# Kernel tuning notes

Hardware: AMD Instinct MI355X
Metric: run time of the kernel (lower is better)

Reference implementation:

```python
import jax, jax.numpy as jnp
import numpy as np

N_EXPERTS = 64
TOPK = 4
DIM = 2048
B_T = 8192


def setup_inputs() -> dict:
    key = jax.random.key(0)
    k1, k2 = jax.random.split(key)
    x = jax.random.normal(k1, (B_T, DIM), jnp.float32)
    W = jax.random.normal(k2, (N_EXPERTS, DIM), jnp.float32) * 0.02  # nn.Linear weight (out, in)
    router_bias = jnp.zeros((N_EXPERTS,), jnp.float32)  # registered buffer, init zeros
    return {"x": x, "W": W, "router_bias": router_bias, "token_capacity": 3072}


def _route(x, W, router_bias, token_capacity):
    """Faithful serial greedy capacity-aware routing.

    Replicates the torch nested loop (k-major, token-minor order):
      - per step, pick argmax over the token's (mutated) logits among experts
        with remaining capacity;
      - full experts whose logit exceeds the chosen one get permanently set
        to -inf in that token's logit row (exactly what the inner while-style
        loop does);
      - if no expert has capacity, selected stays -1, weight 0, and the whole
        row becomes -inf (torch sets the top expert to -inf n_experts times).
    """
    logits0 = x @ W.T + router_bias                       # (N, E)
    scores = jax.nn.softmax(logits0, axis=-1)             # (N, E)
    cap = token_capacity // TOPK                          # python int
    remaining0 = jnp.full((N_EXPERTS,), float(cap), jnp.float32)
    N = x.shape[0]
    NEG = jnp.float32(-jnp.inf)

    def step(carry, i):
        logits, remaining = carry
        b = i % N                                         # token index (k-major order)
        row = logits[b]                                   # (E,)
        masked = jnp.where(remaining > 0, row, NEG)
        chosen = jnp.argmax(masked)
        ok = remaining[chosen] > 0                        # False only if all experts full
        sel = jnp.where(ok, chosen, -1).astype(jnp.int32)
        w = jnp.where(ok, scores[b, chosen], jnp.float32(0.0))
        full = remaining <= 0
        cval = row[chosen]
        # full experts 'above' the chosen one were visited and zapped to -inf
        new_row = jnp.where(ok,
                            jnp.where(full & (row > cval), NEG, row),
                            jnp.full_like(row, NEG))
        logits = logits.at[b].set(new_row)
        remaining = remaining.at[chosen].add(jnp.where(ok, jnp.float32(-1.0), jnp.float32(0.0)))
        return (logits, remaining), (sel, w)

    (_, _), (sel_f, w_f) = jax.lax.scan(step, (logits0, remaining0),
                                        jnp.arange(TOPK * N))
    selected = sel_f.reshape(TOPK, N).T                   # (N, TOPK)
    weights = w_f.reshape(TOPK, N).T                      # (N, TOPK)
    weights = weights / (weights.sum(axis=-1, keepdims=True) + 1e-8)
    return selected, weights


def reference(x, W, router_bias, token_capacity):
    return _route(x, W, router_bias, token_capacity)
```

## Files before the change

### kernel.cpp

```cpp
#include <hip/hip_runtime.h>
#include <math.h>

#define N_TOK 8192
#define DIM   2048
#define NE    64
#define TOPK  4
#define THETA 2e-3f
#define TPB2  16
#define NBLK  (N_TOK / TPB2)
#define RSTR  260

typedef short bf16x8 __attribute__((ext_vector_type(8)));
typedef float f32x4  __attribute__((ext_vector_type(4)));

#define OFF_LOGITS 0
#define OFF_MAXV   (OFF_LOGITS + N_TOK * NE)
#define OFF_DENOM  (OFF_MAXV + N_TOK)
#define OFF_W1     (OFF_DENOM + N_TOK)
#define OFF_C1     (OFF_W1 + N_TOK)
#define OFF_NFLAG  (OFF_C1 + N_TOK)
#define OFF_FLAGL  (OFF_NFLAG + 64)
#define OFF_WH     (OFF_FLAGL + N_TOK)
#define OFF_WL     (OFF_WH + NE * DIM / 2)
#define OFF_WT     (OFF_WL + NE * DIM / 2)
#define OFF_WTMP   (OFF_WT + NE * DIM)

__device__ inline void cvt2(float a, float b, unsigned& hi, unsigned& lo) {
    const unsigned ua = __float_as_uint(a), ub = __float_as_uint(b);
    hi = __builtin_amdgcn_perm(ub, ua, 0x07060302u);
    const float ra = a - __uint_as_float(ua & 0xFFFF0000u);
    const float rb = b - __uint_as_float(ub & 0xFFFF0000u);
    lo = __builtin_amdgcn_perm(__float_as_uint(rb), __float_as_uint(ra), 0x07060302u);
}

union FragU { unsigned u[4]; bf16x8 v; uint4 q; };

__device__ inline void make_frags(const float4& p, const float4& q,
                                  bf16x8& hi, bf16x8& lo) {
    FragU H, L;
    cvt2(p.x, p.y, H.u[0], L.u[0]);
    cvt2(p.z, p.w, H.u[1], L.u[1]);
    cvt2(q.x, q.y, H.u[2], L.u[2]);
    cvt2(q.z, q.w, H.u[3], L.u[3]);
    hi = H.v; lo = L.v;
}

__global__ __launch_bounds__(256)
void k_wc(const float* __restrict__ W, unsigned short* __restrict__ wh2,
          unsigned short* __restrict__ wl2, float* __restrict__ wt,
          int* __restrict__ nflag) {
    const int t = blockIdx.x * 256 + threadIdx.x;
    if (t == 0) nflag[0] = 0;
    const int l  = t & 63;
    const int grp = t >> 6;
    const int nt = grp & 3;
    const int kc = grp >> 2;
    const int e  = nt * 16 + (l & 15);
    const int k0 = kc * 32 + (l >> 4) * 8;

    const float4 p = *reinterpret_cast<const float4*>(W + (size_t)e * DIM + k0);
    const float4 q = *reinterpret_cast<const float4*>(W + (size_t)e * DIM + k0 + 4);
    FragU H, L;
    cvt2(p.x, p.y, H.u[0], L.u[0]);
    cvt2(p.z, p.w, H.u[1], L.u[1]);
    cvt2(q.x, q.y, H.u[2], L.u[2]);
    cvt2(q.z, q.w, H.u[3], L.u[3]);
    const size_t off = (size_t)grp * 512 + l * 8;
    *reinterpret_cast<uint4*>(wh2 + off) = H.q;
    *reinterpret_cast<uint4*>(wl2 + off) = L.q;

    wt[(size_t)(k0 + 0) * NE + e] = p.x;
    wt[(size_t)(k0 + 1) * NE + e] = p.y;
    wt[(size_t)(k0 + 2) * NE + e] = p.z;
    wt[(size_t)(k0 + 3) * NE + e] = p.w;
    wt[(size_t)(k0 + 4) * NE + e] = q.x;
    wt[(size_t)(k0 + 5) * NE + e] = q.y;
    wt[(size_t)(k0 + 6) * NE + e] = q.z;
    wt[(size_t)(k0 + 7) * NE + e] = q.w;
}

__global__ __launch_bounds__(512, 4)
void k_main(const float* __restrict__ x, const unsigned short* __restrict__ wh2,
            const unsigned short* __restrict__ wl2, const float* __restrict__ bias,
            float* __restrict__ logits, float* __restrict__ maxv,
            float* __restrict__ denomv, float* __restrict__ w1f,
            int* __restrict__ c1, int* __restrict__ nflag, int* __restrict__ flagl) {
    __shared__ __align__(16) float xs[2][TPB2 * RSTR];
    __shared__ float red[8][TPB2][68];
    __shared__ float lbuf[TPB2][68];

    const int tid = threadIdx.x;
    const int w   = tid >> 6;
    const int l   = tid & 63;
    const int t0  = blockIdx.x * TPB2;
    const int m   = l & 15;
    const int g   = l >> 4;

    const float* xrow0 = x + (size_t)(t0 + 2 * w) * DIM + l * 4;
    const float* xrow1 = x + (size_t)(t0 + 2 * w + 1) * DIM + l * 4;
    float* st0 = &xs[0][(2 * w) * RSTR + l * 4];
    float* st1 = &xs[0][(2 * w + 1) * RSTR + l * 4];
    const int xs1off = TPB2 * RSTR;

    const unsigned short* bh = wh2 + (size_t)w * 2048 + l * 8;
    const unsigned short* bl = wl2 + (size_t)w * 2048 + l * 8;

    f32x4 accA[4], accB[4];
    #pragma unroll
    for (int nt = 0; nt < 4; ++nt)
        #pragma unroll
        for (int r = 0; r < 4; ++r) { accA[nt][r] = 0.0f; accB[nt][r] = 0.0f; }

    {
        const float4 r0 = *reinterpret_cast<const float4*>(xrow0);
        const float4 r1 = *reinterpret_cast<const float4*>(xrow1);
        *reinterpret_cast<float4*>(st0) = r0;
        *reinterpret_cast<float4*>(st1) = r1;
    }
    uint4 BH[2][4], BL[2][4];
    #pragma unroll
    for (int nt = 0; nt < 4; ++nt) {
        BH[0][nt] = *reinterpret_cast<const uint4*>(bh + nt * 512);
        BL[0][nt] = *reinterpret_cast<const uint4*>(bl + nt * 512);
    }
    __syncthreads();

    const int aoff = m * RSTR + w * 32 + g * 8;

    #pragma unroll
    for (int win = 0; win < 8; ++win) {
        const int cur = win & 1, nxt = cur ^ 1;
        float4 nx0, nx1;
        if (win < 7) {
            nx0 = *reinterpret_cast<const float4*>(xrow0 + (win + 1) * 256);
            nx1 = *reinterpret_cast<const float4*>(xrow1 + (win + 1) * 256);
            #pragma unroll
            for (int nt = 0; nt < 4; ++nt) {
                BH[nxt][nt] = *reinterpret_cast<const uint4*>(
                    bh + (size_t)(win + 1) * 16384 + nt * 512);
                BL[nxt][nt] = *reinterpret_cast<const uint4*>(
                    bl + (size_t)(win + 1) * 16384 + nt * 512);
            }
        }

        const float4 p = *reinterpret_cast<const float4*>(&xs[0][cur * xs1off + aoff]);
        const float4 q = *reinterpret_cast<const float4*>(&xs[0][cur * xs1off + aoff + 4]);
        bf16x8 ah, al;
        make_frags(p, q, ah, al);

        #pragma unroll
        for (int nt = 0; nt < 4; ++nt) {
            FragU b; b.q = BH[cur][nt];
            accA[nt] = __builtin_amdgcn_mfma_f32_16x16x32_bf16(ah, b.v, accA[nt], 0, 0, 0);
            accB[nt] = __builtin_amdgcn_mfma_f32_16x16x32_bf16(al, b.v, accB[nt], 0, 0, 0);
        }
        #pragma unroll
        for (int nt = 0; nt < 4; ++nt) {
            FragU b; b.q = BL[cur][nt];
            accB[nt] = __builtin_amdgcn_mfma_f32_16x16x32_bf16(ah, b.v, accB[nt], 0, 0, 0);
        }

        if (win < 7) {
            *reinterpret_cast<float4*>(st0 + nxt * xs1off) = nx0;
            *reinterpret_cast<float4*>(st1 + nxt * xs1off) = nx1;
        }
        __syncthreads();
    }

    #pragma unroll
    for (int nt = 0; nt < 4; ++nt)
        #pragma unroll
        for (int r = 0; r < 4; ++r)
            red[w][g * 4 + r][nt * 16 + m] = accA[nt][r] + accB[nt][r];
    __syncthreads();

    for (int e2 = tid; e2 < TPB2 * NE; e2 += 512) {
        const int t = e2 >> 6, e = e2 & 63;
        float s = red[0][t][e];
        #pragma unroll
        for (int ww = 1; ww < 8; ++ww) s += red[ww][t][e];
        s += bias[e];
        logits[(size_t)(t0 + t) * NE + e] = s;
        lbuf[t][e] = s;
    }
    __syncthreads();

    #pragma unroll
    for (int tt = 0; tt < 2; ++tt) {
        const int t = w * 2 + tt;
        const float lv = lbuf[t][l];
        float v1 = lv; int i1 = l; float v2 = -INFINITY;
        #pragma unroll
        for (int off = 32; off; off >>= 1) {
            const float ov1 = __shfl_xor(v1, off);
            const int   oi1 = __shfl_xor(i1, off);
            const float ov2 = __shfl_xor(v2, off);
            if (ov1 > v1 || (ov1 == v1 && oi1 < i1)) {
                v2 = fmaxf(v1, ov2); v1 = ov1; i1 = oi1;
            } else {
                v2 = fmaxf(v2, ov1);
            }
        }
        float s = expf(lv - v1);
        #pragma unroll
        for (int off = 32; off; off >>= 1) s += __shfl_xor(s, off);
        if (l == 0) {
            const int row = t0 + t;
            maxv[row]   = v1;
            denomv[row] = s;
            c1[row]     = i1;
            w1f[row]    = 1.0f / s;
            if (v1 - v2 < THETA) {
                const int ix = atomicAdd(nflag, 1);
                flagl[ix] = row;
            }
        }
    }
}

__global__ __launch_bounds__(256)
void k_exact(const int* __restrict__ nflag, const int* __restrict__ flagl,
             const float* __restrict__ x, const float* __restrict__ wt,
             const float* __restrict__ bias, float* __restrict__ logits,
             float* __restrict__ maxv, float* __restrict__ denomv,
             float* __restrict__ w1f, int* __restrict__ c1) {
    __shared__ float part[4][68];
    const int n   = nflag[0];
    const int tid = threadIdx.x;
    const int w   = tid >> 6, l = tid & 63;
    for (int i = blockIdx.x; i < n; i += 64) {
        const int t = flagl[i];
        const float* xr = x + (size_t)t * DIM + w * 512;
        const float* wb = wt + (size_t)(w * 512) * NE + l;
        float a = 0.0f;
        for (int k = 0; k < 512; k += 4) {
            const float4 xv = *reinterpret_cast<const float4*>(xr + k);
            a = fmaf(xv.x, wb[(size_t)(k + 0) * NE], a);
            a = fmaf(xv.y, wb[(size_t)(k + 1) * NE], a);
            a = fmaf(xv.z, wb[(size_t)(k + 2) * NE], a);
            a = fmaf(xv.w, wb[(size_t)(k + 3) * NE], a);
        }
        part[w][l] = a;
        __syncthreads();
        if (w == 0) {
            float lg = bias[l];
            #pragma unroll
            for (int s = 0; s < 4; ++s) lg += part[s][l];
            logits[(size_t)t * NE + l] = lg;
            float v = lg; int idx = l;
            #pragma unroll
            for (int off = 32; off; off >>= 1) {
                const float ov = __shfl_xor(v, off);
                const int   oi = __shfl_xor(idx, off);
                if (ov > v || (ov == v && oi < idx)) { v = ov; idx = oi; }
            }
            float p = expf(lg - v);
            #pragma unroll
            for (int off = 32; off; off >>= 1) p += __shfl_xor(p, off);
            if (l == 0) {
                maxv[t]   = v;
                denomv[t] = p;
                c1[t]     = idx;
                w1f[t]    = 1.0f / p;
            }
        }
        __syncthreads();
    }
}

__global__ __launch_bounds__(256)
void k_decide(const int* __restrict__ c1, const float* __restrict__ w1,
              const float* __restrict__ logits, const float* __restrict__ maxv,
              const float* __restrict__ denomv, const int* __restrict__ tc,
              float* __restrict__ out, float* __restrict__ wtmp) {
    __shared__ int hist[NE];
    __shared__ int flagS;
    const int tid = threadIdx.x;
    if (tid < NE) hist[tid] = 0;
    __syncthreads();
    for (int i = tid; i < N_TOK; i += 256) atomicAdd(&hist[c1[i]], 1);
    __syncthreads();
    const int cap = tc[0] / TOPK;
    if (tid < NE) {
        const bool bad = (TOPK * hist[tid] > cap);
        const unsigned long long mm = __ballot(bad);
        if (tid == 0) flagS = (mm == 0ull) ? 1 : 0;
    }
    __syncthreads();

    if (flagS) {
        const int b = blockIdx.x * 256 + tid;
        const float se = (float)c1[b];
        const float wv = w1[b];
        const float wn = wv / (4.0f * wv + 1e-8f);
        *reinterpret_cast<float4*>(out + (size_t)b * 4) = make_float4(se, se, se, se);
        *reinterpret_cast<float4*>(out + (size_t)N_TOK * TOPK + (size_t)b * 4) =
            make_float4(wn, wn, wn, wn);
        return;
    }

    if (blockIdx.x != 0) return;
    if (tid < 64) {
        const int e = tid;
        int rem = cap;
        for (int k = 0; k < TOPK; ++k) {
            for (int b = 0; b < N_TOK; ++b) {
                const float lg = logits[(size_t)b * NE + e];
                float v = (rem > 0) ? lg : -INFINITY;
                int idx = e;
                #pragma unroll
                for (int off = 32; off; off >>= 1) {
                    const float ov = __shfl_xor(v, off);
                    const int   oi = __shfl_xor(idx, off);
                    if (ov > v || (ov == v && oi < idx)) { v = ov; idx = oi; }
                }
                const bool ok = (v != -INFINITY);
                if (ok && e == idx) rem -= 1;
                const float lc = __shfl(lg, idx);
                if (e == 0) {
                    out[(size_t)b * TOPK + k]  = ok ? (float)idx : -1.0f;
                    wtmp[(size_t)b * TOPK + k] = ok ? expf(lc - maxv[b]) / denomv[b] : 0.0f;
                }
            }
        }
    }
    __syncthreads();
    for (int b = tid; b < N_TOK; b += 256) {
        const float w0 = wtmp[b * 4 + 0], w1_ = wtmp[b * 4 + 1];
        const float w2 = wtmp[b * 4 + 2], w3 = wtmp[b * 4 + 3];
        const float s = ((w0 + w1_) + w2) + w3 + 1e-8f;
        out[N_TOK * TOPK + b * 4 + 0] = w0 / s;
        out[N_TOK * TOPK + b * 4 + 1] = w1_ / s;
        out[N_TOK * TOPK + b * 4 + 2] = w2 / s;
        out[N_TOK * TOPK + b * 4 + 3] = w3 / s;
    }
}

extern "C" void kernel_launch(void* const* d_in, const int* in_sizes, int n_in,
                              void* d_out, int out_size, void* d_ws, size_t ws_size,
                              hipStream_t stream) {
    const float* x    = (const float*)d_in[0];
    const float* W    = (const float*)d_in[1];
    const float* bias = (const float*)d_in[2];
    const int*   tc   = (const int*)d_in[3];

    float* ws       = (float*)d_ws;
    float* logits   = ws + OFF_LOGITS;
    float* maxv     = ws + OFF_MAXV;
    float* denomv   = ws + OFF_DENOM;
    float* w1f      = ws + OFF_W1;
    int*   c1       = (int*)(ws + OFF_C1);
    int*   nflag    = (int*)(ws + OFF_NFLAG);
    int*   flagl    = (int*)(ws + OFF_FLAGL);
    unsigned short* wh2 = (unsigned short*)(ws + OFF_WH);
    unsigned short* wl2 = (unsigned short*)(ws + OFF_WL);
    float* wt       = ws + OFF_WT;
    float* wtmp     = ws + OFF_WTMP;
    float* out      = (float*)d_out;

    k_wc<<<NE * DIM / 8 / 256, 256, 0, stream>>>(W, wh2, wl2, wt, nflag);
    k_main<<<NBLK, 512, 0, stream>>>(x, wh2, wl2, bias, logits, maxv, denomv,
                                     w1f, c1, nflag, flagl);
    k_exact<<<64, 256, 0, stream>>>(nflag, flagl, x, wt, bias, logits,
                                    maxv, denomv, w1f, c1);
    k_decide<<<N_TOK / 256, 256, 0, stream>>>(c1, w1f, logits, maxv, denomv,
                                              tc, out, wtmp);
}
```

Baseline: 130.9 us.

## Fuse exact recompute of near-tie tokens and expert histogram into main kernel

The separate k_exact kernel, which recomputed logits in fp32 for tokens whose top-2 gap fell below a threshold, is removed. That recompute now runs inside k_main per block, using a block-local flag list and all 8 waves. k_main also builds the per-expert top-1 histogram with padded global atomics, so k_decide no longer rescans c1 per block. This drops one launch and a redundant histogram pass in every decide block. In exchange, blocks that contain flagged tokens take longer and k_main carries more shared memory and code.

```diff
diff --git a/kernel.cpp b/kernel.cpp
--- a/kernel.cpp
+++ b/kernel.cpp
@@ -9,6 +9,7 @@
 #define TPB2  16
 #define NBLK  (N_TOK / TPB2)
 #define RSTR  260
+#define HSTR  16
 
 typedef short bf16x8 __attribute__((ext_vector_type(8)));
 typedef float f32x4  __attribute__((ext_vector_type(4)));
@@ -18,9 +19,8 @@
 #define OFF_DENOM  (OFF_MAXV + N_TOK)
 #define OFF_W1     (OFF_DENOM + N_TOK)
 #define OFF_C1     (OFF_W1 + N_TOK)
-#define OFF_NFLAG  (OFF_C1 + N_TOK)
-#define OFF_FLAGL  (OFF_NFLAG + 64)
-#define OFF_WH     (OFF_FLAGL + N_TOK)
+#define OFF_HIST   (OFF_C1 + N_TOK)
+#define OFF_WH     (OFF_HIST + NE * HSTR)
 #define OFF_WL     (OFF_WH + NE * DIM / 2)
 #define OFF_WT     (OFF_WL + NE * DIM / 2)
 #define OFF_WTMP   (OFF_WT + NE * DIM)
@@ -48,9 +48,9 @@
 __global__ __launch_bounds__(256)
 void k_wc(const float* __restrict__ W, unsigned short* __restrict__ wh2,
           unsigned short* __restrict__ wl2, float* __restrict__ wt,
-          int* __restrict__ nflag) {
+          int* __restrict__ hist) {
     const int t = blockIdx.x * 256 + threadIdx.x;
-    if (t == 0) nflag[0] = 0;
+    if (t < NE * HSTR) hist[t] = 0;
     const int l  = t & 63;
     const int grp = t >> 6;
     const int nt = grp & 3;
@@ -82,12 +82,16 @@
 __global__ __launch_bounds__(512, 4)
 void k_main(const float* __restrict__ x, const unsigned short* __restrict__ wh2,
             const unsigned short* __restrict__ wl2, const float* __restrict__ bias,
+            const float* __restrict__ wt,
             float* __restrict__ logits, float* __restrict__ maxv,
             float* __restrict__ denomv, float* __restrict__ w1f,
-            int* __restrict__ c1, int* __restrict__ nflag, int* __restrict__ flagl) {
+            int* __restrict__ c1, int* __restrict__ hist) {
     __shared__ __align__(16) float xs[2][TPB2 * RSTR];
     __shared__ float red[8][TPB2][68];
     __shared__ float lbuf[TPB2][68];
+    __shared__ int   selS[TPB2];
+    __shared__ short flagIdx[TPB2];
+    __shared__ int   flagCnt;
 
     const int tid = threadIdx.x;
     const int w   = tid >> 6;
@@ -95,6 +99,8 @@
     const int t0  = blockIdx.x * TPB2;
     const int m   = l & 15;
     const int g   = l >> 4;
+
+    if (tid == 0) flagCnt = 0;
 
     const float* xrow0 = x + (size_t)(t0 + 2 * w) * DIM + l * 4;
     const float* xrow1 = x + (size_t)(t0 + 2 * w + 1) * DIM + l * 4;
@@ -210,43 +216,42 @@
             denomv[row] = s;
             c1[row]     = i1;
             w1f[row]    = 1.0f / s;
+            selS[t]     = i1;
             if (v1 - v2 < THETA) {
-                const int ix = atomicAdd(nflag, 1);
-                flagl[ix] = row;
-            }
-        }
-    }
-}
-
-__global__ __launch_bounds__(256)
-void k_exact(const int* __restrict__ nflag, const int* __restrict__ flagl,
-             const float* __restrict__ x, const float* __restrict__ wt,
-             const float* __restrict__ bias, float* __restrict__ logits,
-             float* __restrict__ maxv, float* __restrict__ denomv,
-             float* __restrict__ w1f, int* __restrict__ c1) {
-    __shared__ float part[4][68];
-    const int n   = nflag[0];
-    const int tid = threadIdx.x;
-    const int w   = tid >> 6, l = tid & 63;
-    for (int i = blockIdx.x; i < n; i += 64) {
-        const int t = flagl[i];
-        const float* xr = x + (size_t)t * DIM + w * 512;
-        const float* wb = wt + (size_t)(w * 512) * NE + l;
-        float a = 0.0f;
-        for (int k = 0; k < 512; k += 4) {
-            const float4 xv = *reinterpret_cast<const float4*>(xr + k);
-            a = fmaf(xv.x, wb[(size_t)(k + 0) * NE], a);
-            a = fmaf(xv.y, wb[(size_t)(k + 1) * NE], a);
-            a = fmaf(xv.z, wb[(size_t)(k + 2) * NE], a);
-            a = fmaf(xv.w, wb[(size_t)(k + 3) * NE], a);
-        }
-        part[w][l] = a;
+                const int ix = atomicAdd(&flagCnt, 1);
+                flagIdx[ix] = (short)t;
+            }
+        }
+    }
+    __syncthreads();
+
+    const int nf = flagCnt;
+    for (int fi = 0; fi < nf; ++fi) {
+        const int tl  = flagIdx[fi];
+        const int row = t0 + tl;
+        const float* xr = x + (size_t)row * DIM + w * 256;
+        const float* wb = wt + (size_t)(w * 256) * NE + l;
+        float a0 = 0.0f, a1 = 0.0f;
+        #pragma unroll 4
+        for (int k = 0; k < 256; k += 8) {
+            const float4 x0 = *reinterpret_cast<const float4*>(xr + k);
+            const float4 x1 = *reinterpret_cast<const float4*>(xr + k + 4);
+            a0 = fmaf(x0.x, wb[(size_t)(k + 0) * NE], a0);
+            a0 = fmaf(x0.y, wb[(size_t)(k + 1) * NE], a0);
+            a0 = fmaf(x0.z, wb[(size_t)(k + 2) * NE], a0);
+            a0 = fmaf(x0.w, wb[(size_t)(k + 3) * NE], a0);
+            a1 = fmaf(x1.x, wb[(size_t)(k + 4) * NE], a1);
+            a1 = fmaf(x1.y, wb[(size_t)(k + 5) * NE], a1);
+            a1 = fmaf(x1.z, wb[(size_t)(k + 6) * NE], a1);
+            a1 = fmaf(x1.w, wb[(size_t)(k + 7) * NE], a1);
+        }
+        red[w][0][l] = a0 + a1;
         __syncthreads();
         if (w == 0) {
             float lg = bias[l];
             #pragma unroll
-            for (int s = 0; s < 4; ++s) lg += part[s][l];
-            logits[(size_t)t * NE + l] = lg;
+            for (int s2 = 0; s2 < 8; ++s2) lg += red[s2][0][l];
+            logits[(size_t)row * NE + l] = lg;
             float v = lg; int idx = l;
             #pragma unroll
             for (int off = 32; off; off >>= 1) {
@@ -258,31 +263,35 @@
             #pragma unroll
             for (int off = 32; off; off >>= 1) p += __shfl_xor(p, off);
             if (l == 0) {
-                maxv[t]   = v;
-                denomv[t] = p;
-                c1[t]     = idx;
-                w1f[t]    = 1.0f / p;
+                maxv[row]   = v;
+                denomv[row] = p;
+                c1[row]     = idx;
+                w1f[row]    = 1.0f / p;
+                selS[tl]    = idx;
             }
         }
         __syncthreads();
     }
+
+    if (w == 0) {
+        int cnt = 0;
+        #pragma unroll
+        for (int t = 0; t < TPB2; ++t) cnt += (selS[t] == l) ? 1 : 0;
+        if (cnt) atomicAdd(&hist[l * HSTR], cnt);
+    }
 }
 
 __global__ __launch_bounds__(256)
-void k_decide(const int* __restrict__ c1, const float* __restrict__ w1,
-              const float* __restrict__ logits, const float* __restrict__ maxv,
-              const float* __restrict__ denomv, const int* __restrict__ tc,
-              float* __restrict__ out, float* __restrict__ wtmp) {
-    __shared__ int hist[NE];
+void k_decide(const int* __restrict__ hist, const int* __restrict__ c1,
+              const float* __restrict__ w1, const float* __restrict__ logits,
+              const float* __restrict__ maxv, const float* __restrict__ denomv,
+              const int* __restrict__ tc, float* __restrict__ out,
+              float* __restrict__ wtmp) {
     __shared__ int flagS;
     const int tid = threadIdx.x;
-    if (tid < NE) hist[tid] = 0;
-    __syncthreads();
-    for (int i = tid; i < N_TOK; i += 256) atomicAdd(&hist[c1[i]], 1);
-    __syncthreads();
     const int cap = tc[0] / TOPK;
     if (tid < NE) {
-        const bool bad = (TOPK * hist[tid] > cap);
+        const bool bad = (TOPK * hist[tid * HSTR] > cap);
         const unsigned long long mm = __ballot(bad);
         if (tid == 0) flagS = (mm == 0ull) ? 1 : 0;
     }
@@ -350,19 +359,16 @@
     float* denomv   = ws + OFF_DENOM;
     float* w1f      = ws + OFF_W1;
     int*   c1       = (int*)(ws + OFF_C1);
-    int*   nflag    = (int*)(ws + OFF_NFLAG);
-    int*   flagl    = (int*)(ws + OFF_FLAGL);
+    int*   hist     = (int*)(ws + OFF_HIST);
     unsigned short* wh2 = (unsigned short*)(ws + OFF_WH);
     unsigned short* wl2 = (unsigned short*)(ws + OFF_WL);
     float* wt       = ws + OFF_WT;
     float* wtmp     = ws + OFF_WTMP;
     float* out      = (float*)d_out;
 
-    k_wc<<<NE * DIM / 8 / 256, 256, 0, stream>>>(W, wh2, wl2, wt, nflag);
-    k_main<<<NBLK, 512, 0, stream>>>(x, wh2, wl2, bias, logits, maxv, denomv,
-                                     w1f, c1, nflag, flagl);
-    k_exact<<<64, 256, 0, stream>>>(nflag, flagl, x, wt, bias, logits,
-                                    maxv, denomv, w1f, c1);
-    k_decide<<<N_TOK / 256, 256, 0, stream>>>(c1, w1f, logits, maxv, denomv,
+    k_wc<<<NE * DIM / 8 / 256, 256, 0, stream>>>(W, wh2, wl2, wt, hist);
+    k_main<<<NBLK, 512, 0, stream>>>(x, wh2, wl2, bias, wt, logits, maxv, denomv,
+                                     w1f, c1, hist);
+    k_decide<<<N_TOK / 256, 256, 0, stream>>>(hist, c1, w1f, logits, maxv, denomv,
                                               tc, out, wtmp);
 }
```

New measurement: 131.3 us. Within noise of the previous version (+0.3%).
